# Optimization experiments

Measured on AMD Instinct MI355X. Metric: run time of the kernel, lower is better.

Reference implementation:

```python
import jax
import jax.numpy as jnp
from jax import lax
import numpy as np

S_DIM = 8
K = 2
TAU = 0.01
MAX_ITER = 100
TOL = 1e-3


def setup_inputs() -> dict:
    key = jax.random.key(0)
    s = jax.random.normal(key, (4_000_000, S_DIM), dtype=jnp.float32)
    return {"s": s}


def _compute_threshold(s, k, tau):
    # init: (k+1)-th largest element per row, matching sorted_s[:, -k-1]
    sorted_s = jnp.sort(s, axis=-1)
    theta0 = sorted_s[:, -k - 1][:, None]  # (B, 1)

    def step(carry, _):
        theta, done = carry
        m = jax.nn.sigmoid((s - theta) / tau)                 # (B, S)
        f = m.sum(axis=-1, keepdims=True) - k                 # (B, 1)
        # torch breaks BEFORE the update when mean(f) < tol
        new_done = done | (jnp.mean(f) < TOL)
        df = -(1.0 / tau) * (m * (1.0 - m)).sum(axis=-1, keepdims=True)
        theta_new = jnp.where(new_done, theta, theta - f / df)
        return (theta_new, new_done), None

    (theta, _), _ = lax.scan(step, (theta0, jnp.array(False)), None, length=MAX_ITER)
    return theta


def reference(s) -> jnp.ndarray:
    theta = _compute_threshold(s, K, TAU)
    return jax.nn.sigmoid((s - theta) / TAU)
```

## Files before the change

### kernel.cpp

```cpp
#include <hip/hip_runtime.h>


__global__ __launch_bounds__(256) void smooth_topk_kernel(
    const float* __restrict__ s, float* __restrict__ out, int nrows) {
  int row = blockIdx.x * blockDim.x + threadIdx.x;
  if (row >= nrows) return;

  const float4* sp = reinterpret_cast<const float4*>(s) + (size_t)row * 2;
  float4 a4 = sp[0];
  float4 b4 = sp[1];

  const float C = 144.26950408889634f;
  float vc[8] = {a4.x * C, a4.y * C, a4.z * C, a4.w * C,
                 b4.x * C, b4.y * C, b4.z * C, b4.w * C};

  float a = fmaxf(vc[0], vc[1]), b = fminf(vc[0], vc[1]);
  float c = fmaxf(vc[2], vc[3]), d = fminf(vc[2], vc[3]);
  float minac = fminf(a, c);
  float p1 = fmaxf(a, c);
  float p2 = fmaxf(minac, fmaxf(b, d));
  float p3 = __builtin_amdgcn_fmed3f(b, d, minac);
  float e = fmaxf(vc[4], vc[5]), f_ = fminf(vc[4], vc[5]);
  float g = fmaxf(vc[6], vc[7]), h = fminf(vc[6], vc[7]);
  float mineg = fminf(e, g);
  float q1 = fmaxf(e, g);
  float q2 = fmaxf(mineg, fmaxf(f_, h));
  float q3 = __builtin_amdgcn_fmed3f(f_, h, mineg);
  float t2 = fmaxf(fminf(p1, q1), fmaxf(p2, q2));
  float t3 = fmaxf(fmaxf(fminf(p2, q1), fminf(p1, q2)), fmaxf(p3, q3));

  float phi = 0.5f * (t2 + t3);
  const float lo = t3 - 4.33f;
  const float hi = t2 + 4.33f;

#pragma unroll
  for (int it = 0; it < 3; ++it) {
    float f = -2.0f;
    float gg = 0.0f;
#pragma unroll
    for (int i = 0; i < 8; ++i) {
      float ex = __builtin_amdgcn_exp2f(phi - vc[i]);
      float m = __builtin_amdgcn_rcpf(1.0f + ex);
      f += m;
      gg = fmaf(m, 1.0f - m, gg);
    }
    float step = f * 1.4426950408889634f * __builtin_amdgcn_rcpf(fmaxf(gg, 1e-12f));
    phi = fminf(fmaxf(phi + step, lo), hi);
  }

  float o[8];
#pragma unroll
  for (int i = 0; i < 8; ++i) {
    float ex = __builtin_amdgcn_exp2f(phi - vc[i]);
    o[i] = __builtin_amdgcn_rcpf(1.0f + ex);
  }
  float4* op = reinterpret_cast<float4*>(out) + (size_t)row * 2;
  op[0] = make_float4(o[0], o[1], o[2], o[3]);
  op[1] = make_float4(o[4], o[5], o[6], o[7]);
}

extern "C" void kernel_launch(void* const* d_in, const int* in_sizes, int n_in,
                              void* d_out, int out_size, void* d_ws, size_t ws_size,
                              hipStream_t stream) {
  const float* s = (const float*)d_in[0];
  float* out = (float*)d_out;
  int nrows = in_sizes[0] / 8;
  int block = 256;
  int grid = (nrows + block - 1) / block;
  smooth_topk_kernel<<<grid, block, 0, stream>>>(s, out, nrows);
}
```

Baseline: 220.9 us.

## Split each row across two lanes with shuffle-based reductions

Each thread now handles half a row (one float4) instead of a full row, and pairs of lanes exchange partial top-3 values and the per-iteration sum and derivative through xor shuffles. This doubles thread count and makes every global load and store a single contiguous float4 per lane, which improves coalescing and latency hiding for this memory-bound kernel. In exchange it adds shuffle instructions and duplicates the Newton-step scalar math across both lanes. The early return relies on the total number of float4s being even so that paired lanes stay together.

Result: faster. 212.0 us (-4.1%).

```diff
diff --git a/kernel.cpp b/kernel.cpp
--- a/kernel.cpp
+++ b/kernel.cpp
@@ -2,30 +2,26 @@
 
 
 __global__ __launch_bounds__(256) void smooth_topk_kernel(
-    const float* __restrict__ s, float* __restrict__ out, int nrows) {
-  int row = blockIdx.x * blockDim.x + threadIdx.x;
-  if (row >= nrows) return;
-
-  const float4* sp = reinterpret_cast<const float4*>(s) + (size_t)row * 2;
-  float4 a4 = sp[0];
-  float4 b4 = sp[1];
+    const float* __restrict__ s, float* __restrict__ out, int nhalf) {
+  int gid = blockIdx.x * blockDim.x + threadIdx.x;
+  if (gid >= nhalf) return;
 
   const float C = 144.26950408889634f;
-  float vc[8] = {a4.x * C, a4.y * C, a4.z * C, a4.w * C,
-                 b4.x * C, b4.y * C, b4.z * C, b4.w * C};
 
-  float a = fmaxf(vc[0], vc[1]), b = fminf(vc[0], vc[1]);
-  float c = fmaxf(vc[2], vc[3]), d = fminf(vc[2], vc[3]);
-  float minac = fminf(a, c);
+  float4 v4 = reinterpret_cast<const float4*>(s)[gid];
+  float v0 = v4.x * C, v1 = v4.y * C, v2 = v4.z * C, v3 = v4.w * C;
+
+  float a = fmaxf(v0, v1), b = fminf(v0, v1);
+  float c = fmaxf(v2, v3), d = fminf(v2, v3);
+  float mn = fminf(a, c);
   float p1 = fmaxf(a, c);
-  float p2 = fmaxf(minac, fmaxf(b, d));
-  float p3 = __builtin_amdgcn_fmed3f(b, d, minac);
-  float e = fmaxf(vc[4], vc[5]), f_ = fminf(vc[4], vc[5]);
-  float g = fmaxf(vc[6], vc[7]), h = fminf(vc[6], vc[7]);
-  float mineg = fminf(e, g);
-  float q1 = fmaxf(e, g);
-  float q2 = fmaxf(mineg, fmaxf(f_, h));
-  float q3 = __builtin_amdgcn_fmed3f(f_, h, mineg);
+  float p2 = fmaxf(mn, fmaxf(b, d));
+  float p3 = __builtin_amdgcn_fmed3f(b, d, mn);
+
+  float q1 = __shfl_xor(p1, 1, 64);
+  float q2 = __shfl_xor(p2, 1, 64);
+  float q3 = __shfl_xor(p3, 1, 64);
+
   float t2 = fmaxf(fminf(p1, q1), fmaxf(p2, q2));
   float t3 = fmaxf(fmaxf(fminf(p2, q1), fminf(p1, q2)), fmaxf(p3, q3));
 
@@ -35,28 +31,29 @@
 
 #pragma unroll
   for (int it = 0; it < 3; ++it) {
-    float f = -2.0f;
-    float gg = 0.0f;
-#pragma unroll
-    for (int i = 0; i < 8; ++i) {
-      float ex = __builtin_amdgcn_exp2f(phi - vc[i]);
-      float m = __builtin_amdgcn_rcpf(1.0f + ex);
-      f += m;
-      gg = fmaf(m, 1.0f - m, gg);
-    }
-    float step = f * 1.4426950408889634f * __builtin_amdgcn_rcpf(fmaxf(gg, 1e-12f));
+    float e0 = __builtin_amdgcn_exp2f(phi - v0);
+    float e1 = __builtin_amdgcn_exp2f(phi - v1);
+    float e2 = __builtin_amdgcn_exp2f(phi - v2);
+    float e3 = __builtin_amdgcn_exp2f(phi - v3);
+    float m0 = __builtin_amdgcn_rcpf(1.0f + e0);
+    float m1 = __builtin_amdgcn_rcpf(1.0f + e1);
+    float m2 = __builtin_amdgcn_rcpf(1.0f + e2);
+    float m3 = __builtin_amdgcn_rcpf(1.0f + e3);
+    float fh = (m0 + m1) + (m2 + m3);
+    float gh = fmaf(m0, 1.0f - m0, fmaf(m1, 1.0f - m1,
+               fmaf(m2, 1.0f - m2, m3 * (1.0f - m3))));
+    float f = (fh + __shfl_xor(fh, 1, 64)) - 2.0f;
+    float g = gh + __shfl_xor(gh, 1, 64);
+    float step = f * 1.4426950408889634f * __builtin_amdgcn_rcpf(fmaxf(g, 1e-12f));
     phi = fminf(fmaxf(phi + step, lo), hi);
   }
 
-  float o[8];
-#pragma unroll
-  for (int i = 0; i < 8; ++i) {
-    float ex = __builtin_amdgcn_exp2f(phi - vc[i]);
-    o[i] = __builtin_amdgcn_rcpf(1.0f + ex);
-  }
-  float4* op = reinterpret_cast<float4*>(out) + (size_t)row * 2;
-  op[0] = make_float4(o[0], o[1], o[2], o[3]);
-  op[1] = make_float4(o[4], o[5], o[6], o[7]);
+  float4 o;
+  o.x = __builtin_amdgcn_rcpf(1.0f + __builtin_amdgcn_exp2f(phi - v0));
+  o.y = __builtin_amdgcn_rcpf(1.0f + __builtin_amdgcn_exp2f(phi - v1));
+  o.z = __builtin_amdgcn_rcpf(1.0f + __builtin_amdgcn_exp2f(phi - v2));
+  o.w = __builtin_amdgcn_rcpf(1.0f + __builtin_amdgcn_exp2f(phi - v3));
+  reinterpret_cast<float4*>(out)[gid] = o;
 }
 
 extern "C" void kernel_launch(void* const* d_in, const int* in_sizes, int n_in,
@@ -64,8 +61,8 @@
                               hipStream_t stream) {
   const float* s = (const float*)d_in[0];
   float* out = (float*)d_out;
-  int nrows = in_sizes[0] / 8;
+  int nhalf = in_sizes[0] / 4;
   int block = 256;
-  int grid = (nrows + block - 1) / block;
-  smooth_topk_kernel<<<grid, block, 0, stream>>>(s, out, nrows);
+  int grid = (nhalf + block - 1) / block;
+  smooth_topk_kernel<<<grid, block, 0, stream>>>(s, out, nhalf);
 }
```
